# Optimization experiments

Measured on AMD Instinct MI355X. Metric: run time of the kernel, lower is better.

Reference implementation:

```python
import jax, jax.numpy as jnp
import numpy as np

N, Q, CC = 8, 300, 92          # batch, queries, logit channels (91 classes + 1 objectness)
CF, HF, WF = 2048, 42, 42      # backbone feature map
M, TOPK = 20, 5                # GT boxes per image, pseudo-unknown top-k
NUM_CLASSES = 91
L_CLS, L_IOU, L_L1 = 2.0, 2.0, 5.0
NEG = -1e11


def cxcywh_to_xyxy(bx):
    cx, cy, bw, bh = bx[..., 0], bx[..., 1], bx[..., 2], bx[..., 3]
    return jnp.stack([cx - bw / 2, cy - bh / 2, cx + bw / 2, cy + bh / 2], -1)


def setup_inputs() -> dict:
    key = jax.random.key(0)
    ks = jax.random.split(key, 6)
    h = w = 1333
    img_features = jax.random.normal(ks[0], (N, CF, HF, WF), jnp.float32)
    pred_logits = jax.random.normal(ks[1], (N, Q, CC), jnp.float32)
    pred_boxes = jax.random.uniform(ks[2], (N, Q, 4), jnp.float32, 0.05, 0.95)
    tgt_labels = jax.random.randint(ks[3], (N, M), 0, NUM_CLASSES - 1).astype(jnp.int32)
    u = jax.random.uniform(ks[4], (N, M, 4), jnp.float32)
    # GT boxes in pixel cxcywh (bbox_normalize divides by image size)
    tgt_boxes = jnp.stack([u[..., 0] * w, u[..., 1] * h,
                           u[..., 2] * 0.3 * w + 2.0, u[..., 3] * 0.3 * h + 2.0], -1)
    perm = jax.vmap(lambda k: jax.random.permutation(k, Q))(jax.random.split(ks[5], N))
    query_idx = perm[:, :M].astype(jnp.int32)          # unique matched query per target
    tgt_idx = jnp.tile(jnp.arange(M, dtype=jnp.int32), (N, 1))
    return dict(img_features=img_features, pred_logits=pred_logits, pred_boxes=pred_boxes,
                tgt_labels=tgt_labels, tgt_boxes=tgt_boxes, query_idx=query_idx,
                tgt_idx=tgt_idx, h=h, w=w)


def _loss(img_features, pred_logits, pred_boxes, tgt_boxes, tgt_labels, query_idx, tgt_idx, h, w):
    b = jnp.arange(N)[:, None]
    scale = jnp.array([w, h, w, h], jnp.float32)
    out_prob = jnp.concatenate([jax.nn.softmax(pred_logits[..., :-1], -1),
                                jax.nn.sigmoid(pred_logits[..., -1:])], -1)  # [N,Q,92]
    matched_mask = jnp.zeros((N, Q), bool).at[b, query_idx].set(True)

    # --- per-query crop-mean pooling: bilinear upsample once + summed-area table ---
    mean_feat = jnp.mean(img_features, 1)                                  # [N,HF,WF]
    up = jax.vmap(lambda f: jax.image.resize(f, (h, w), 'bilinear'))(mean_feat)  # [N,h,w]
    sat = jnp.pad(jnp.cumsum(jnp.cumsum(up, 1), 2), ((0, 0), (1, 0), (1, 0)))    # [N,h+1,w+1]
    bb = cxcywh_to_xyxy(pred_boxes) * scale                                # pixel xyxy
    x1 = jnp.clip(bb[..., 0].astype(jnp.int32), 0, w)
    y1 = jnp.clip(bb[..., 1].astype(jnp.int32), 0, h)
    x2 = jnp.clip(bb[..., 2].astype(jnp.int32), 0, w)
    y2 = jnp.clip(bb[..., 3].astype(jnp.int32), 0, h)
    cnt = jnp.maximum(y2 - y1, 0) * jnp.maximum(x2 - x1, 0)
    x2e, y2e = jnp.maximum(x2, x1), jnp.maximum(y2, y1)
    boxsum = sat[b, y2e, x2e] - sat[b, y1, x2e] - sat[b, y2e, x1] + sat[b, y1, x1]
    means = jnp.where(cnt > 0, boxsum / jnp.maximum(cnt, 1), NEG)          # empty crop -> -1e11 (nan case)
    means = jnp.where(matched_mask, NEG, means)                            # matched queries excluded
    _, topk_idx = jax.lax.top_k(means, TOPK)                               # [N,TOPK]
    topk_mask = jnp.zeros((N, Q), bool).at[b, topk_idx].set(True)

    # --- matched terms ---
    tgt_cls = tgt_labels[b, tgt_idx]                                       # [N,M]
    tgt_bb = tgt_boxes[b, tgt_idx] / scale                                 # bbox_normalize
    q_cls = out_prob[b, query_idx, :NUM_CLASSES]                           # probs; CE re-applies log_softmax (faithful)
    q_obj = out_prob[b, query_idx, -1]
    q_bb = pred_boxes[b, query_idx]
    logp = jax.nn.log_softmax(q_cls, -1)
    ce_matched = -jnp.mean(jnp.take_along_axis(logp, tgt_cls[..., None].astype(jnp.int32), -1)[..., 0], 1)
    bce_matched = -jnp.mean(jnp.maximum(jnp.log(q_obj), -100.0), 1)
    l1 = jnp.sqrt(jnp.sum((q_bb - tgt_bb) ** 2, (1, 2)))                   # torch.dist (Frobenius)
    a, t = cxcywh_to_xyxy(q_bb), cxcywh_to_xyxy(tgt_bb)
    ix1 = jnp.maximum(a[..., 0], t[..., 0]); iy1 = jnp.maximum(a[..., 1], t[..., 1])
    ix2 = jnp.minimum(a[..., 2], t[..., 2]); iy2 = jnp.minimum(a[..., 3], t[..., 3])
    inter = jnp.clip(ix2 - ix1, 0.0) * jnp.clip(iy2 - iy1, 0.0)
    area = lambda z: (z[..., 2] - z[..., 0]) * (z[..., 3] - z[..., 1])
    iou = inter / (area(a) + area(t) - inter + 1e-9)
    iou_loss = jnp.sum(1.0 - iou, 1)

    # --- pseudo-unknown terms ---
    pk_cls = out_prob[b, topk_idx, :NUM_CLASSES]
    ce_pseudo = -jnp.mean(jax.nn.log_softmax(pk_cls, -1)[..., NUM_CLASSES - 1], 1)
    pk_obj = out_prob[b, topk_idx, -1]
    bce_topk = -jnp.mean(jnp.maximum(jnp.log(pk_obj), -100.0), 1)
    rest = (~matched_mask) & (~topk_mask)                                  # setdiff(other, topk)
    neglog1m = -jnp.maximum(jnp.log1p(-out_prob[..., -1]), -100.0)
    bce_rest = jnp.sum(jnp.where(rest, neglog1m, 0.0), 1) / jnp.maximum(jnp.sum(rest, 1), 1)

    cls_loss = jnp.sum(ce_matched + ce_pseudo)
    obj_loss = jnp.sum(bce_matched + bce_rest + bce_topk)
    return (cls_loss * L_CLS + obj_loss * L_CLS
            + jnp.sum(iou_loss) * L_IOU + jnp.sum(l1) * L_L1)


def reference(img_features, pred_logits, pred_boxes, tgt_labels, tgt_boxes, query_idx, tgt_idx, h, w):
    return _loss(img_features, pred_logits, pred_boxes, tgt_boxes, tgt_labels, query_idx, tgt_idx, h, w)
```

## Files before the change

### kernel.cpp

```cpp
#include <hip/hip_runtime.h>
#include <math.h>

#define NB 8
#define QN 300
#define CCH 92
#define NCLS 91
#define CFCH 2048
#define HFD 42
#define MT 20
#define TOPK5 5
#define DIM 1333
#define DIMF 1333.0f
#define PIX (HFD*HFD)
#define PIX4 (PIX/4)
#define CHUNKS 32
#define CPC (CFCH/CHUNKS)
#define NEGV -100000000000.0f

#define PART_BLOCKS (NB*CHUNKS*2)
#define CUM_TOTAL   (2*(DIM+1)*HFD)
#define CUM_BLOCKS  ((CUM_TOTAL + 255)/256)
#define STAT_BLOCKS ((NB*QN)/4)

__device__ __forceinline__ float bilin_w(int i, int j, float s) {
    float sf = ((float)i + 0.5f) * s - 0.5f;
    if (sf <= 0.f)                return (j == 0) ? 1.f : 0.f;
    if (sf >= (float)(HFD - 1))   return (j == HFD - 1) ? 1.f : 0.f;
    int j0 = (int)sf;
    float fr = sf - (float)j0;
    if (j == j0)     return 1.f - fr;
    if (j == j0 + 1) return fr;
    return 0.f;
}

__device__ __forceinline__ float wave_sum(float v) {
    for (int off = 32; off; off >>= 1) v += __shfl_down(v, off);
    return v;
}

__global__ __launch_bounds__(256) void stage_a(
        const float4* __restrict__ img, float4* __restrict__ part,
        float* __restrict__ CX, float* __restrict__ CY,
        const float* __restrict__ logits, const float* __restrict__ boxes,
        const int* __restrict__ query_idx, const int* __restrict__ tgt_idx,
        const int* __restrict__ tgt_labels, const float* __restrict__ tgt_boxes,
        float* __restrict__ ls2a, float* __restrict__ p90a,
        float* __restrict__ ptga, float* __restrict__ nobja,
        float* __restrict__ n1ma, float* __restrict__ l1a,
        float* __restrict__ ioua, float* __restrict__ out) {
    int blk = blockIdx.x;
    if (blk == 0 && threadIdx.x == 0) out[0] = 0.f;
    if (blk < PART_BLOCKS) {
        int tile = blk & 1;
        int chunk = (blk >> 1) & (CHUNKS - 1);
        int b = blk >> 6;
        int f = tile * 256 + threadIdx.x;
        if (f >= PIX4) return;
        const float4* p = img + (size_t)(b * CFCH + chunk * CPC) * PIX4 + f;
        float x = 0.f, y = 0.f, z = 0.f, w = 0.f;
#pragma unroll 8
        for (int k = 0; k < CPC; ++k) {
            float4 v = p[(size_t)k * PIX4];
            x += v.x; y += v.y; z += v.z; w += v.w;
        }
        float4 o; o.x = x; o.y = y; o.z = z; o.w = w;
        part[(size_t)(blk >> 1) * PIX4 + f] = o;
    } else if (blk < PART_BLOCKS + CUM_BLOCKS) {
        int idx = (blk - PART_BLOCKS) * 256 + threadIdx.x;
        const int total = (DIM + 1) * HFD;
        int t = idx / total;
        if (t >= 2) return;
        int rem = idx - t * total;
        int X = rem / HFD;
        int j = rem - X * HFD;
        const float s = (float)HFD / DIMF;
        int i0 = max(0, (int)floorf(((float)j - 0.5f) / s - 0.5f) - 2);
        int i1 = min(DIM, (int)ceilf(((float)j + 1.5f) / s - 0.5f) + 2);
        int hi = min(X, i1);
        float acc = 0.f;
        for (int i = i0; i < hi; ++i) acc += bilin_w(i, j, s);
        float* C = t ? CY : CX;
        C[X * HFD + j] = acc;
    } else {
        int gw = (blk - PART_BLOCKS - CUM_BLOCKS) * 4 + (threadIdx.x >> 6);
        int lane = threadIdx.x & 63;
        int b = gw / QN, q = gw - b * QN;
        int mpos = -1;
#pragma unroll
        for (int m = 0; m < MT; ++m) if (query_idx[b * MT + m] == q) mpos = m;
        const float* L = logits + (size_t)gw * CCH;
        float c0 = L[lane];
        float e1 = (lane < CCH - 64) ? L[lane + 64] : 0.f;
        bool has_c1 = (lane < NCLS - 64);
        float mx = fmaxf(c0, has_c1 ? e1 : -3.4e38f);
        for (int off = 32; off; off >>= 1) mx = fmaxf(mx, __shfl_xor(mx, off));
        float se = expf(c0 - mx) + (has_c1 ? expf(e1 - mx) : 0.f);
        for (int off = 32; off; off >>= 1) se += __shfl_xor(se, off);
        float inv = 1.f / se;
        float s2 = expf(expf(c0 - mx) * inv) + (has_c1 ? expf(expf(e1 - mx) * inv) : 0.f);
        for (int off = 32; off; off >>= 1) s2 += __shfl_xor(s2, off);
        float ls2 = logf(s2);
        float l90  = __shfl(e1, 26);
        float lobj = __shfl(e1, 27);
        float p90 = expf(l90 - mx) * inv;
        float sg = 1.f / (1.f + expf(-lobj));
        float nobj = -fmaxf(logf(sg), -100.f);
        float n1m  = -fmaxf(log1pf(-sg), -100.f);

        float ptg = 0.f, l1 = 0.f, iouc = 0.f;
        if (mpos >= 0) {
            const float* bx = boxes + (size_t)gw * 4;
            float cx = bx[0], cy = bx[1], bw = bx[2], bh = bx[3];
            int ti = tgt_idx[b * MT + mpos];
            int tc = tgt_labels[b * MT + ti];
            ptg = expf(L[tc] - mx) * inv;
            const float* tb = tgt_boxes + (size_t)(b * MT + ti) * 4;
            float t0 = tb[0] / DIMF, t1 = tb[1] / DIMF, t2 = tb[2] / DIMF, t3 = tb[3] / DIMF;
            float d0 = cx - t0, d1 = cy - t1, d2 = bw - t2, d3 = bh - t3;
            l1 = d0 * d0 + d1 * d1 + d2 * d2 + d3 * d3;
            float ax1 = cx - bw * 0.5f, ay1 = cy - bh * 0.5f;
            float ax2 = cx + bw * 0.5f, ay2 = cy + bh * 0.5f;
            float tx1 = t0 - t2 * 0.5f, ty1 = t1 - t3 * 0.5f;
            float tx2 = t0 + t2 * 0.5f, ty2 = t1 + t3 * 0.5f;
            float ix1 = fmaxf(ax1, tx1), iy1 = fmaxf(ay1, ty1);
            float ix2 = fminf(ax2, tx2), iy2 = fminf(ay2, ty2);
            float inter = fmaxf(ix2 - ix1, 0.f) * fmaxf(iy2 - iy1, 0.f);
            float aa = (ax2 - ax1) * (ay2 - ay1), at = (tx2 - tx1) * (ty2 - ty1);
            float iou = inter / (aa + at - inter + 1e-9f);
            iouc = 1.f - iou;
        }
        if (lane == 0) {
            ls2a[gw] = ls2; p90a[gw] = p90; ptga[gw] = ptg;
            nobja[gw] = nobj; n1ma[gw] = n1m; l1a[gw] = l1; ioua[gw] = iouc;
        }
    }
}

__global__ __launch_bounds__(1024) void fuse_b(
        const float* __restrict__ part, const float* __restrict__ boxes,
        const int* __restrict__ query_idx,
        const float* __restrict__ CX, const float* __restrict__ CY,
        const float* __restrict__ ls2a, const float* __restrict__ p90a,
        const float* __restrict__ ptga, const float* __restrict__ nobja,
        const float* __restrict__ n1ma, const float* __restrict__ l1a,
        const float* __restrict__ ioua, float* __restrict__ out) {
    int b = blockIdx.x, tid = threadIdx.x;
    int wid = tid >> 6, lane = tid & 63;
    __shared__ float s_mf[PIX];
    __shared__ float s_d[16][84];
    __shared__ float s_means[QN];
    __shared__ unsigned char s_matched[QN], s_sel[QN];
    __shared__ float s_red[16];
    __shared__ int   s_redi[16];
    __shared__ float s_acc[16][8];

    const float* pp = part + (size_t)b * CHUNKS * PIX;
    for (int pix = tid; pix < PIX; pix += 1024) {
        float acc = 0.f;
#pragma unroll
        for (int c = 0; c < CHUNKS; ++c) acc += pp[c * PIX + pix];
        s_mf[pix] = acc * (1.0f / (float)CFCH);
    }
    for (int q = tid; q < QN; q += 1024) { s_matched[q] = 0; s_sel[q] = 0; }
    __syncthreads();
    if (tid < MT) s_matched[query_idx[b * MT + tid]] = 1;
    __syncthreads();

    float r_mf[28]; int r_rc[28];
#pragma unroll
    for (int i = 0; i < 28; ++i) {
        int pix = lane + (i << 6);
        if (pix < PIX) {
            int row = pix / HFD, col = pix - row * HFD;
            r_rc[i] = (row << 7) | col;
            r_mf[i] = s_mf[pix];
        } else { r_rc[i] = 0; r_mf[i] = 0.f; }
    }

    for (int q = wid; q < QN; q += 16) {
        const float* bx = boxes + (size_t)(b * QN + q) * 4;
        float cx = bx[0], cy = bx[1], bw = bx[2], bh = bx[3];
        int x1 = min(max((int)((cx - bw * 0.5f) * DIMF), 0), DIM);
        int y1 = min(max((int)((cy - bh * 0.5f) * DIMF), 0), DIM);
        int x2 = min(max((int)((cx + bw * 0.5f) * DIMF), 0), DIM);
        int y2 = min(max((int)((cy + bh * 0.5f) * DIMF), 0), DIM);
        int x2e = max(x2, x1), y2e = max(y2, y1);
        int cnt = max(y2 - y1, 0) * max(x2 - x1, 0);
        float val = NEGV;
        if (!s_matched[q] && cnt > 0) {
            if (lane < HFD) {
                s_d[wid][lane]      = CY[y2e * HFD + lane] - CY[y1 * HFD + lane];
                s_d[wid][42 + lane] = CX[x2e * HFD + lane] - CX[x1 * HFD + lane];
            }
            float acc = 0.f;
#pragma unroll
            for (int i = 0; i < 28; ++i) {
                int rc = r_rc[i];
                acc += s_d[wid][rc >> 7] * s_d[wid][42 + (rc & 127)] * r_mf[i];
            }
            acc = wave_sum(acc);
            val = acc / (float)cnt;
        }
        if (lane == 0) s_means[q] = val;
    }
    __syncthreads();

    for (int r = 0; r < TOPK5; ++r) {
        float bv = -3.4e38f; int bi = QN;
        if (tid < QN && !s_sel[tid]) {
            bv = s_means[tid]; bi = tid;
        }
        for (int off = 32; off; off >>= 1) {
            float ov = __shfl_down(bv, off); int oi = __shfl_down(bi, off);
            if (ov > bv || (ov == bv && oi < bi)) { bv = ov; bi = oi; }
        }
        if (lane == 0) { s_red[wid] = bv; s_redi[wid] = bi; }
        __syncthreads();
        if (tid == 0) {
            float fv = s_red[0]; int fi = s_redi[0];
            for (int k = 1; k < 16; ++k)
                if (s_red[k] > fv || (s_red[k] == fv && s_redi[k] < fi)) { fv = s_red[k]; fi = s_redi[k]; }
            s_sel[fi] = 1;
        }
        __syncthreads();
    }

    float a0 = 0, a1 = 0, a2 = 0, a3 = 0, a4 = 0, a5 = 0, a6 = 0; int rc = 0;
    if (tid < QN) {
        int g = b * QN + tid;
        if (s_matched[tid]) {
            a0 += ls2a[g] - ptga[g];
            a1 += nobja[g];
            a2 += l1a[g];
            a3 += ioua[g];
        } else if (s_sel[tid]) {
            a4 += ls2a[g] - p90a[g];
            a5 += nobja[g];
        } else {
            a6 += n1ma[g]; rc++;
        }
    }
    a0 = wave_sum(a0); a1 = wave_sum(a1); a2 = wave_sum(a2); a3 = wave_sum(a3);
    a4 = wave_sum(a4); a5 = wave_sum(a5); a6 = wave_sum(a6);
    float rcf = wave_sum((float)rc);
    if (lane == 0) {
        s_acc[wid][0] = a0; s_acc[wid][1] = a1; s_acc[wid][2] = a2; s_acc[wid][3] = a3;
        s_acc[wid][4] = a4; s_acc[wid][5] = a5; s_acc[wid][6] = a6; s_acc[wid][7] = rcf;
    }
    __syncthreads();
    if (tid == 0) {
        float A[8];
        for (int k = 0; k < 8; ++k) {
            float t = 0.f;
            for (int w = 0; w < 16; ++w) t += s_acc[w][k];
            A[k] = t;
        }
        float ce_matched = A[0] / (float)MT;
        float bce_matched = A[1] / (float)MT;
        float l1 = sqrtf(A[2]);
        float iou_loss = A[3];
        float ce_pseudo = A[4] / (float)TOPK5;
        float bce_topk = A[5] / (float)TOPK5;
        int rcT = (int)(A[7] + 0.5f);
        float bce_rest = A[6] / (float)max(rcT, 1);
        float total = 2.f * (ce_matched + ce_pseudo)
                    + 2.f * (bce_matched + bce_rest + bce_topk)
                    + 2.f * iou_loss + 5.f * l1;
        atomicAdd(out, total);
    }
}

extern "C" void kernel_launch(void* const* d_in, const int* in_sizes, int n_in,
                              void* d_out, int out_size, void* d_ws, size_t ws_size,
                              hipStream_t stream) {
    const float* img        = (const float*)d_in[0];
    const float* logits     = (const float*)d_in[1];
    const float* boxes      = (const float*)d_in[2];
    const int*   tgt_labels = (const int*)d_in[3];
    const float* tgt_boxes  = (const float*)d_in[4];
    const int*   query_idx  = (const int*)d_in[5];
    const int*   tgt_idx    = (const int*)d_in[6];

    float* ws    = (float*)d_ws;
    float* part  = ws;
    float* CX    = part + (size_t)NB * CHUNKS * PIX;
    float* CY    = CX + (size_t)(DIM + 1) * HFD;
    float* ls2a  = CY + (size_t)(DIM + 1) * HFD;
    float* p90a  = ls2a + NB * QN;
    float* ptga  = p90a + NB * QN;
    float* nobja = ptga + NB * QN;
    float* n1ma  = nobja + NB * QN;
    float* l1a   = n1ma + NB * QN;
    float* ioua  = l1a + NB * QN;

    stage_a<<<PART_BLOCKS + CUM_BLOCKS + STAT_BLOCKS, 256, 0, stream>>>(
        (const float4*)img, (float4*)part, CX, CY, logits, boxes,
        query_idx, tgt_idx, tgt_labels, tgt_boxes,
        ls2a, p90a, ptga, nobja, n1ma, l1a, ioua, (float*)d_out);
    fuse_b<<<NB, 1024, 0, stream>>>(part, boxes, query_idx, CX, CY,
                                    ls2a, p90a, ptga, nobja, n1ma, l1a, ioua,
                                    (float*)d_out);
}
```

Baseline: 227.7 us.

## Spread box-mean computation across many blocks with last-block top-k finalize

The second kernel ran only 8 blocks, one per image, each looping over 300 queries. Now 600 blocks each handle 4 queries and write their means to global memory. An atomic counter per image picks the last finishing block, which performs a wave-level bitonic top-8 merge to select the top-5 and then does the final reduction. Each block now recomputes the 32-chunk channel sum into shared memory, which adds redundant global reads. It also relies on threadfence and atomic ordering for correctness.

```diff
diff --git a/kernel.cpp b/kernel.cpp
--- a/kernel.cpp
+++ b/kernel.cpp
@@ -21,6 +21,8 @@
 #define CUM_TOTAL   (2*(DIM+1)*HFD)
 #define CUM_BLOCKS  ((CUM_TOTAL + 255)/256)
 #define STAT_BLOCKS ((NB*QN)/4)
+#define BPB 75
+#define BM_BLOCKS (NB*BPB)
 
 __device__ __forceinline__ float bilin_w(int i, int j, float s) {
     float sf = ((float)i + 0.5f) * s - 0.5f;
@@ -38,6 +40,9 @@
     return v;
 }
 
+#define BETTER(av,ai,bv,bi) ((av) > (bv) || ((av) == (bv) && (ai) < (bi)))
+#define CEM(aV,aI,bV,bI) { if (BETTER(bV,bI,aV,aI)) { float _tv=aV; aV=bV; bV=_tv; int _ti=aI; aI=bI; bI=_ti; } }
+
 __global__ __launch_bounds__(256) void stage_a(
         const float4* __restrict__ img, float4* __restrict__ part,
         float* __restrict__ CX, float* __restrict__ CY,
@@ -47,9 +52,13 @@
         float* __restrict__ ls2a, float* __restrict__ p90a,
         float* __restrict__ ptga, float* __restrict__ nobja,
         float* __restrict__ n1ma, float* __restrict__ l1a,
-        float* __restrict__ ioua, float* __restrict__ out) {
+        float* __restrict__ ioua, int* __restrict__ cnt,
+        float* __restrict__ out) {
     int blk = blockIdx.x;
-    if (blk == 0 && threadIdx.x == 0) out[0] = 0.f;
+    if (blk == 0) {
+        if (threadIdx.x == 0) out[0] = 0.f;
+        if (threadIdx.x < NB) cnt[threadIdx.x] = 0;
+    }
     if (blk < PART_BLOCKS) {
         int tile = blk & 1;
         int chunk = (blk >> 1) & (CHUNKS - 1);
@@ -136,58 +145,60 @@
     }
 }
 
-__global__ __launch_bounds__(1024) void fuse_b(
+__global__ __launch_bounds__(256) void box_fin(
         const float* __restrict__ part, const float* __restrict__ boxes,
         const int* __restrict__ query_idx,
         const float* __restrict__ CX, const float* __restrict__ CY,
         const float* __restrict__ ls2a, const float* __restrict__ p90a,
         const float* __restrict__ ptga, const float* __restrict__ nobja,
         const float* __restrict__ n1ma, const float* __restrict__ l1a,
-        const float* __restrict__ ioua, float* __restrict__ out) {
-    int b = blockIdx.x, tid = threadIdx.x;
+        const float* __restrict__ ioua,
+        float* __restrict__ means, int* __restrict__ cnt,
+        float* __restrict__ out) {
+    int blk = blockIdx.x, tid = threadIdx.x;
     int wid = tid >> 6, lane = tid & 63;
+    int b = blk / BPB, loc = blk - b * BPB;
+
     __shared__ float s_mf[PIX];
-    __shared__ float s_d[16][84];
-    __shared__ float s_means[QN];
-    __shared__ unsigned char s_matched[QN], s_sel[QN];
-    __shared__ float s_red[16];
-    __shared__ int   s_redi[16];
-    __shared__ float s_acc[16][8];
-
-    const float* pp = part + (size_t)b * CHUNKS * PIX;
-    for (int pix = tid; pix < PIX; pix += 1024) {
-        float acc = 0.f;
-#pragma unroll
-        for (int c = 0; c < CHUNKS; ++c) acc += pp[c * PIX + pix];
-        s_mf[pix] = acc * (1.0f / (float)CFCH);
-    }
-    for (int q = tid; q < QN; q += 1024) { s_matched[q] = 0; s_sel[q] = 0; }
+    __shared__ float s_d[4][84];
+    __shared__ unsigned char s_matched[QN];
+    __shared__ int s_flag;
+    __shared__ int s_top[TOPK5];
+    __shared__ float s_acc[4][8];
+
+    const float4* pp = (const float4*)(part + (size_t)b * CHUNKS * PIX);
+    float4* s_mf4 = (float4*)s_mf;
+    for (int p4 = tid; p4 < PIX4; p4 += 256) {
+        float x = 0.f, y = 0.f, z = 0.f, w = 0.f;
+#pragma unroll
+        for (int c = 0; c < CHUNKS; ++c) {
+            float4 v = pp[c * PIX4 + p4];
+            x += v.x; y += v.y; z += v.z; w += v.w;
+        }
+        float4 o;
+        o.x = x * (1.f / (float)CFCH); o.y = y * (1.f / (float)CFCH);
+        o.z = z * (1.f / (float)CFCH); o.w = w * (1.f / (float)CFCH);
+        s_mf4[p4] = o;
+    }
+    for (int q = tid; q < QN; q += 256) s_matched[q] = 0;
+    if (tid == 0) s_flag = 0;
     __syncthreads();
     if (tid < MT) s_matched[query_idx[b * MT + tid]] = 1;
     __syncthreads();
 
-    float r_mf[28]; int r_rc[28];
-#pragma unroll
-    for (int i = 0; i < 28; ++i) {
-        int pix = lane + (i << 6);
-        if (pix < PIX) {
-            int row = pix / HFD, col = pix - row * HFD;
-            r_rc[i] = (row << 7) | col;
-            r_mf[i] = s_mf[pix];
-        } else { r_rc[i] = 0; r_mf[i] = 0.f; }
-    }
-
-    for (int q = wid; q < QN; q += 16) {
-        const float* bx = boxes + (size_t)(b * QN + q) * 4;
+    {
+        int q = loc * 4 + wid;
+        int g = b * QN + q;
+        const float* bx = boxes + (size_t)g * 4;
         float cx = bx[0], cy = bx[1], bw = bx[2], bh = bx[3];
         int x1 = min(max((int)((cx - bw * 0.5f) * DIMF), 0), DIM);
         int y1 = min(max((int)((cy - bh * 0.5f) * DIMF), 0), DIM);
         int x2 = min(max((int)((cx + bw * 0.5f) * DIMF), 0), DIM);
         int y2 = min(max((int)((cy + bh * 0.5f) * DIMF), 0), DIM);
         int x2e = max(x2, x1), y2e = max(y2, y1);
-        int cnt = max(y2 - y1, 0) * max(x2 - x1, 0);
+        int boxcnt = max(y2 - y1, 0) * max(x2 - x1, 0);
         float val = NEGV;
-        if (!s_matched[q] && cnt > 0) {
+        if (!s_matched[q] && boxcnt > 0) {
             if (lane < HFD) {
                 s_d[wid][lane]      = CY[y2e * HFD + lane] - CY[y1 * HFD + lane];
                 s_d[wid][42 + lane] = CX[x2e * HFD + lane] - CX[x1 * HFD + lane];
@@ -195,45 +206,81 @@
             float acc = 0.f;
 #pragma unroll
             for (int i = 0; i < 28; ++i) {
-                int rc = r_rc[i];
-                acc += s_d[wid][rc >> 7] * s_d[wid][42 + (rc & 127)] * r_mf[i];
+                int pix = lane + (i << 6);
+                if (pix < PIX) {
+                    int row = pix / HFD;
+                    int col = pix - row * HFD;
+                    acc += s_d[wid][row] * s_d[wid][42 + col] * s_mf[pix];
+                }
             }
             acc = wave_sum(acc);
-            val = acc / (float)cnt;
-        }
-        if (lane == 0) s_means[q] = val;
-    }
-    __syncthreads();
-
-    for (int r = 0; r < TOPK5; ++r) {
-        float bv = -3.4e38f; int bi = QN;
-        if (tid < QN && !s_sel[tid]) {
-            bv = s_means[tid]; bi = tid;
-        }
+            val = acc / (float)boxcnt;
+        }
+        if (lane == 0) means[g] = val;
+    }
+
+    __threadfence();
+    __syncthreads();
+    if (tid == 0) {
+        int old = atomicAdd(&cnt[b], 1);
+        if (old == BPB - 1) s_flag = 1;
+    }
+    __syncthreads();
+    if (!s_flag) return;
+    __threadfence();
+
+    if (wid == 0) {
+        const float SENT = -3.4e38f; const int SENTI = 0x7fffffff;
+        float v0=SENT,v1=SENT,v2=SENT,v3=SENT,v4=SENT,v5=SENT,v6=SENT,v7=SENT;
+        int   i0=SENTI,i1=SENTI,i2=SENTI,i3=SENTI,i4=SENTI,i5=SENTI,i6=SENTI,i7=SENTI;
+#pragma unroll
+        for (int k = 0; k < 5; ++k) {
+            int q = lane + (k << 6);
+            if (q < QN) {
+                float ev = means[b * QN + q]; int ei = q;
+                if (BETTER(ev, ei, v7, i7)) {
+                    v7 = ev; i7 = ei;
+                    CEM(v6,i6,v7,i7); CEM(v5,i5,v6,i6); CEM(v4,i4,v5,i5);
+                    CEM(v3,i3,v4,i4); CEM(v2,i2,v3,i3); CEM(v1,i1,v2,i2);
+                    CEM(v0,i0,v1,i1);
+                }
+            }
+        }
+#pragma unroll
         for (int off = 32; off; off >>= 1) {
-            float ov = __shfl_down(bv, off); int oi = __shfl_down(bi, off);
-            if (ov > bv || (ov == bv && oi < bi)) { bv = ov; bi = oi; }
-        }
-        if (lane == 0) { s_red[wid] = bv; s_redi[wid] = bi; }
-        __syncthreads();
-        if (tid == 0) {
-            float fv = s_red[0]; int fi = s_redi[0];
-            for (int k = 1; k < 16; ++k)
-                if (s_red[k] > fv || (s_red[k] == fv && s_redi[k] < fi)) { fv = s_red[k]; fi = s_redi[k]; }
-            s_sel[fi] = 1;
-        }
-        __syncthreads();
-    }
+            float u0=__shfl_xor(v0,off),u1=__shfl_xor(v1,off),u2=__shfl_xor(v2,off),u3=__shfl_xor(v3,off);
+            float u4=__shfl_xor(v4,off),u5=__shfl_xor(v5,off),u6=__shfl_xor(v6,off),u7=__shfl_xor(v7,off);
+            int   j0=__shfl_xor(i0,off),j1=__shfl_xor(i1,off),j2=__shfl_xor(i2,off),j3=__shfl_xor(i3,off);
+            int   j4=__shfl_xor(i4,off),j5=__shfl_xor(i5,off),j6=__shfl_xor(i6,off),j7=__shfl_xor(i7,off);
+            if (BETTER(u7,j7,v0,i0)) { v0=u7; i0=j7; }
+            if (BETTER(u6,j6,v1,i1)) { v1=u6; i1=j6; }
+            if (BETTER(u5,j5,v2,i2)) { v2=u5; i2=j5; }
+            if (BETTER(u4,j4,v3,i3)) { v3=u4; i3=j4; }
+            if (BETTER(u3,j3,v4,i4)) { v4=u3; i4=j3; }
+            if (BETTER(u2,j2,v5,i5)) { v5=u2; i5=j2; }
+            if (BETTER(u1,j1,v6,i6)) { v6=u1; i6=j1; }
+            if (BETTER(u0,j0,v7,i7)) { v7=u0; i7=j0; }
+            CEM(v0,i0,v4,i4); CEM(v1,i1,v5,i5); CEM(v2,i2,v6,i6); CEM(v3,i3,v7,i7);
+            CEM(v0,i0,v2,i2); CEM(v1,i1,v3,i3); CEM(v4,i4,v6,i6); CEM(v5,i5,v7,i7);
+            CEM(v0,i0,v1,i1); CEM(v2,i2,v3,i3); CEM(v4,i4,v5,i5); CEM(v6,i6,v7,i7);
+        }
+        if (lane == 0) {
+            s_top[0] = i0; s_top[1] = i1; s_top[2] = i2; s_top[3] = i3; s_top[4] = i4;
+        }
+    }
+    __syncthreads();
 
     float a0 = 0, a1 = 0, a2 = 0, a3 = 0, a4 = 0, a5 = 0, a6 = 0; int rc = 0;
-    if (tid < QN) {
-        int g = b * QN + tid;
-        if (s_matched[tid]) {
+    for (int q = tid; q < QN; q += 256) {
+        int g = b * QN + q;
+        bool sel = (q == s_top[0]) | (q == s_top[1]) | (q == s_top[2])
+                 | (q == s_top[3]) | (q == s_top[4]);
+        if (s_matched[q]) {
             a0 += ls2a[g] - ptga[g];
             a1 += nobja[g];
             a2 += l1a[g];
             a3 += ioua[g];
-        } else if (s_sel[tid]) {
+        } else if (sel) {
             a4 += ls2a[g] - p90a[g];
             a5 += nobja[g];
         } else {
@@ -250,11 +297,8 @@
     __syncthreads();
     if (tid == 0) {
         float A[8];
-        for (int k = 0; k < 8; ++k) {
-            float t = 0.f;
-            for (int w = 0; w < 16; ++w) t += s_acc[w][k];
-            A[k] = t;
-        }
+        for (int k = 0; k < 8; ++k)
+            A[k] = s_acc[0][k] + s_acc[1][k] + s_acc[2][k] + s_acc[3][k];
         float ce_matched = A[0] / (float)MT;
         float bce_matched = A[1] / (float)MT;
         float l1 = sqrtf(A[2]);
@@ -285,19 +329,21 @@
     float* part  = ws;
     float* CX    = part + (size_t)NB * CHUNKS * PIX;
     float* CY    = CX + (size_t)(DIM + 1) * HFD;
-    float* ls2a  = CY + (size_t)(DIM + 1) * HFD;
+    float* means = CY + (size_t)(DIM + 1) * HFD;
+    float* ls2a  = means + NB * QN;
     float* p90a  = ls2a + NB * QN;
     float* ptga  = p90a + NB * QN;
     float* nobja = ptga + NB * QN;
     float* n1ma  = nobja + NB * QN;
     float* l1a   = n1ma + NB * QN;
     float* ioua  = l1a + NB * QN;
+    int*   cnt   = (int*)(ioua + NB * QN);
 
     stage_a<<<PART_BLOCKS + CUM_BLOCKS + STAT_BLOCKS, 256, 0, stream>>>(
         (const float4*)img, (float4*)part, CX, CY, logits, boxes,
         query_idx, tgt_idx, tgt_labels, tgt_boxes,
-        ls2a, p90a, ptga, nobja, n1ma, l1a, ioua, (float*)d_out);
-    fuse_b<<<NB, 1024, 0, stream>>>(part, boxes, query_idx, CX, CY,
-                                    ls2a, p90a, ptga, nobja, n1ma, l1a, ioua,
-                                    (float*)d_out);
-}
+        ls2a, p90a, ptga, nobja, n1ma, l1a, ioua, cnt, (float*)d_out);
+    box_fin<<<BM_BLOCKS, 256, 0, stream>>>(part, boxes, query_idx, CX, CY,
+                                           ls2a, p90a, ptga, nobja, n1ma,
+                                           l1a, ioua, means, cnt, (float*)d_out);
+}
```

Measured after the change: 245.6 us. +7.9%, slower.
